# Performance work log

Hardware: AMD Instinct MI355X
Metric: run time of the kernel (lower is better)

Reference implementation:

```python
import jax, jax.numpy as jnp
import numpy as np

D_INNER = 5120
DT_RANK = 160
N_STATE = 16
BATCH = 256


def _softplus_thresh20(x):
    # ttnn.softplus(parameter1=1.0, parameter2=20.0): linear above threshold 20
    return jnp.where(x > 20.0, x, jnp.log1p(jnp.exp(jnp.minimum(x, 20.0))))


def setup_inputs() -> dict:
    key = jax.random.key(0)
    ks = jax.random.split(key, 9)
    x = jax.random.normal(ks[0], (1, 1, BATCH, D_INNER), dtype=jnp.float32)
    # scale weights by 1/sqrt(fan_in) so softplus input is O(1)
    W_dt_low = jax.random.normal(ks[1], (D_INNER, DT_RANK), dtype=jnp.float32) / np.sqrt(D_INNER)
    W_dt = jax.random.normal(ks[2], (DT_RANK, D_INNER), dtype=jnp.float32) / np.sqrt(DT_RANK)
    b_dt = jax.random.normal(ks[3], (D_INNER,), dtype=jnp.float32)
    W_B = jax.random.normal(ks[4], (D_INNER, N_STATE), dtype=jnp.float32) / np.sqrt(D_INNER)
    W_C = jax.random.normal(ks[5], (D_INNER, N_STATE), dtype=jnp.float32) / np.sqrt(D_INNER)
    # A = -exp(A_log): strictly negative, as in the module's preprocess_A
    A = -jnp.exp(0.5 * jax.random.normal(ks[6], (D_INNER, N_STATE), dtype=jnp.float32))
    D = jax.random.normal(ks[7], (D_INNER,), dtype=jnp.float32)
    h0 = 0.1 * jax.random.normal(ks[8], (BATCH, D_INNER, N_STATE), dtype=jnp.float32)
    return {"x": x, "W_dt_low": W_dt_low, "W_dt": W_dt, "b_dt": b_dt,
            "W_B": W_B, "W_C": W_C, "A": A, "D": D, "h0": h0}


def reference(x, W_dt_low, W_dt, b_dt, W_B, W_C, A, D, h0):
    b, d = x.shape[2], x.shape[3]
    xb = x.reshape(b, d)                                  # (B, D)
    # delta = softplus(x @ x_proj_dt @ dt_proj + bias)
    delta = _softplus_thresh20(xb @ W_dt_low @ W_dt + b_dt)   # (B, D)
    Bp = xb @ W_B                                         # (B, N)
    Cp = xb @ W_C                                         # (B, N)
    # discretize: abar = exp(delta * A), bbar = delta * B
    # layout (B, D, N) matches repeat_interleave(delta, n) / repeat(B, d)
    abar = jnp.exp(delta[:, :, None] * A[None, :, :])     # (B, D, N)
    bbar = delta[:, :, None] * Bp[:, None, :]             # (B, D, N)
    h = abar * h0 + bbar * xb[:, :, None]                 # (B, D, N)
    y = jnp.einsum('bdn,bn->bd', h, Cp)                   # reduce over state
    out = xb * D[None, :] + y                             # (B, D)
    return out.reshape(1, 1, b, d)
```

## Files before the change

kernel.cpp:

```cpp
#include <hip/hip_runtime.h>
#include <math.h>

#define D_INNER 5120
#define DT_RANK 160
#define N_STATE 16
#define BATCH   256
#define KTOT    192

#define BGRP    8
#define NBG     (BATCH / BGRP)
#define DDBLK   160
#define NDDB    (D_INNER / DDBLK)
#define SPLIT   32

#define K3_BT   8

#define OFF_T     0
#define SZ_T      (BATCH * KTOT)
#define OFF_P     (OFF_T + SZ_T)
#define SZ_P      (SPLIT * BATCH * KTOT)
#define OFF_SBC   (OFF_P + SZ_P)

__global__ __launch_bounds__(256) void k1_gemm(const float* __restrict__ x,
                                               const float* __restrict__ Wdtlow,
                                               const float* __restrict__ WB,
                                               const float* __restrict__ WC,
                                               float* __restrict__ ws) {
    __shared__ float lds[4 * BGRP * KTOT];
    const int tid  = threadIdx.x;
    const int lane = tid & 63;
    const int wv   = tid >> 6;
    const int b0   = blockIdx.x * BGRP;
    const int ddB  = blockIdx.y * DDBLK;

    float* xs = lds;
    for (int j = tid; j < (BGRP * DDBLK) / 4; j += 256) {
        int i  = j / (DDBLK / 4);
        int c4 = j % (DDBLK / 4);
        float4 v = *(const float4*)(x + (size_t)(b0 + i) * D_INNER + ddB + c4 * 4);
        *(float4*)(xs + i * DDBLK + c4 * 4) = v;
    }
    __syncthreads();

    const int dd0 = wv * 40;
    const float* p0 = Wdtlow + (size_t)(ddB + dd0) * DT_RANK + lane;
    const float* p1 = p0 + 64;
    const float* p2;
    int st2;
    if (lane < 32)      { p2 = p0 + 128;                                          st2 = DT_RANK; }
    else if (lane < 48) { p2 = WB + (size_t)(ddB + dd0) * N_STATE + (lane - 32);  st2 = N_STATE; }
    else                { p2 = WC + (size_t)(ddB + dd0) * N_STATE + (lane - 48);  st2 = N_STATE; }

    float acc0[BGRP], acc1[BGRP], acc2[BGRP];
#pragma unroll
    for (int i = 0; i < BGRP; ++i) { acc0[i] = 0.f; acc1[i] = 0.f; acc2[i] = 0.f; }

#pragma unroll 2
    for (int g = 0; g < 10; ++g) {
        float w0[4], w1[4], w2[4];
#pragma unroll
        for (int u = 0; u < 4; ++u) {
            int dd = g * 4 + u;
            w0[u] = p0[(size_t)dd * DT_RANK];
            w1[u] = p1[(size_t)dd * DT_RANK];
            w2[u] = p2[(size_t)dd * st2];
        }
#pragma unroll
        for (int i = 0; i < BGRP; ++i) {
            float4 xv = *(const float4*)(xs + i * DDBLK + dd0 + g * 4);
            acc0[i] += xv.x * w0[0] + xv.y * w0[1] + xv.z * w0[2] + xv.w * w0[3];
            acc1[i] += xv.x * w1[0] + xv.y * w1[1] + xv.z * w1[2] + xv.w * w1[3];
            acc2[i] += xv.x * w2[0] + xv.y * w2[1] + xv.z * w2[2] + xv.w * w2[3];
        }
    }
    __syncthreads();

#pragma unroll
    for (int i = 0; i < BGRP; ++i) {
        float* r = lds + wv * (BGRP * KTOT) + i * KTOT;
        r[lane]       = acc0[i];
        r[lane + 64]  = acc1[i];
        r[lane + 128] = acc2[i];
    }
    __syncthreads();

    float* P = ws + OFF_P + (size_t)blockIdx.y * (BATCH * KTOT) + (size_t)b0 * KTOT;
#pragma unroll
    for (int r = 0; r < 6; ++r) {
        int idx = tid + r * 256;
        P[idx] = lds[idx] + lds[idx + 1536] + lds[idx + 3072] + lds[idx + 4608];
    }
}

__global__ __launch_bounds__(192) void k2_reduce(float* __restrict__ ws) {
    __shared__ float ts[KTOT];
    const int b   = blockIdx.x;
    const int col = threadIdx.x;
    const float* P = ws + OFF_P + (size_t)b * KTOT + col;
    float a = 0.f;
#pragma unroll
    for (int s = 0; s < SPLIT; ++s) a += P[(size_t)s * (BATCH * KTOT)];
    ws[OFF_T + b * KTOT + col] = a;
    ts[col] = a;
    __syncthreads();
    if (col == 0) {
        float s2 = 0.f;
#pragma unroll
        for (int n = 0; n < N_STATE; ++n) s2 += ts[160 + n] * ts[176 + n];
        ws[OFF_SBC + b] = s2;
    }
}

__global__ __launch_bounds__(256, 4) void k3_fused(const float* __restrict__ Wdt,
                                                   const float* __restrict__ b_dt,
                                                   const float* __restrict__ x,
                                                   const float* __restrict__ A,
                                                   const float* __restrict__ Dv,
                                                   const float* __restrict__ h0,
                                                   const float* __restrict__ ws,
                                                   float* __restrict__ out) {
    const int tid = threadIdx.x;
    const int d   = blockIdx.x * 256 + tid;
    const int b0  = blockIdx.y * K3_BT;
    const float* T  = ws + OFF_T;
    const float* SB = ws + OFF_SBC;

    const float4* hb = (const float4*)(h0 + ((size_t)b0 * D_INNER + d) * N_STATE);
    const size_t  hstride = (size_t)D_INNER * 4;

    float4 hc0 = hb[0], hc1 = hb[1], hc2 = hb[2], hc3 = hb[3];
    const float4* h1p = hb + hstride;
    float4 hn0 = h1p[0], hn1 = h1p[1], hn2 = h1p[2], hn3 = h1p[3];

    float xv[K3_BT];
#pragma unroll
    for (int i = 0; i < K3_BT; ++i) xv[i] = x[(size_t)(b0 + i) * D_INNER + d];

    const float bdt = b_dt[d];
    const float Dd  = Dv[d];
    const float4* a4 = (const float4*)(A + (size_t)d * N_STATE);
    float4 a0 = a4[0], a1 = a4[1], a2 = a4[2], a3 = a4[3];

    float acc[K3_BT] = {0.f, 0.f, 0.f, 0.f, 0.f, 0.f, 0.f, 0.f};
#pragma unroll 4
    for (int k = 0; k < DT_RANK; ++k) {
        float w = Wdt[(size_t)k * D_INNER + d];
#pragma unroll
        for (int i = 0; i < K3_BT; ++i)
            acc[i] += T[(size_t)(b0 + i) * KTOT + k] * w;
    }

#pragma unroll
    for (int i = 0; i < K3_BT; ++i) {
        float4 p0, p1, p2, p3;
        if (i + 2 < K3_BT) {
            const float4* hp = hb + (size_t)(i + 2) * hstride;
            p0 = hp[0]; p1 = hp[1]; p2 = hp[2]; p3 = hp[3];
        }

        const int b = b0 + i;
        const float* Tb = T + (size_t)b * KTOT;

        float v     = acc[i] + bdt;
        float delta = (v > 20.f) ? v : log1pf(__expf(v));
        float sbc   = SB[b];

        float y0, y1, y2, y3;
        y0  = __expf(delta * a0.x) * hc0.x * Tb[176 + 0];
        y0 += __expf(delta * a0.y) * hc0.y * Tb[176 + 1];
        y0 += __expf(delta * a0.z) * hc0.z * Tb[176 + 2];
        y0 += __expf(delta * a0.w) * hc0.w * Tb[176 + 3];
        y1  = __expf(delta * a1.x) * hc1.x * Tb[176 + 4];
        y1 += __expf(delta * a1.y) * hc1.y * Tb[176 + 5];
        y1 += __expf(delta * a1.z) * hc1.z * Tb[176 + 6];
        y1 += __expf(delta * a1.w) * hc1.w * Tb[176 + 7];
        y2  = __expf(delta * a2.x) * hc2.x * Tb[176 + 8];
        y2 += __expf(delta * a2.y) * hc2.y * Tb[176 + 9];
        y2 += __expf(delta * a2.z) * hc2.z * Tb[176 + 10];
        y2 += __expf(delta * a2.w) * hc2.w * Tb[176 + 11];
        y3  = __expf(delta * a3.x) * hc3.x * Tb[176 + 12];
        y3 += __expf(delta * a3.y) * hc3.y * Tb[176 + 13];
        y3 += __expf(delta * a3.z) * hc3.z * Tb[176 + 14];
        y3 += __expf(delta * a3.w) * hc3.w * Tb[176 + 15];

        out[(size_t)b * D_INNER + d] = xv[i] * (Dd + delta * sbc)
                                     + ((y0 + y1) + (y2 + y3));

        if (i < K3_BT - 1) { hc0 = hn0; hc1 = hn1; hc2 = hn2; hc3 = hn3; }
        if (i + 2 < K3_BT) { hn0 = p0;  hn1 = p1;  hn2 = p2;  hn3 = p3;  }
    }
}

extern "C" void kernel_launch(void* const* d_in, const int* in_sizes, int n_in,
                              void* d_out, int out_size, void* d_ws, size_t ws_size,
                              hipStream_t stream) {
    const float* x      = (const float*)d_in[0];
    const float* Wdtlow = (const float*)d_in[1];
    const float* Wdt    = (const float*)d_in[2];
    const float* bdt    = (const float*)d_in[3];
    const float* WB     = (const float*)d_in[4];
    const float* WC     = (const float*)d_in[5];
    const float* A      = (const float*)d_in[6];
    const float* Dv     = (const float*)d_in[7];
    const float* h0     = (const float*)d_in[8];
    float* ws  = (float*)d_ws;
    float* out = (float*)d_out;

    hipLaunchKernelGGL(k1_gemm, dim3(NBG, NDDB), dim3(256), 0, stream,
                       x, Wdtlow, WB, WC, ws);
    hipLaunchKernelGGL(k2_reduce, dim3(BATCH), dim3(192), 0, stream, ws);
    hipLaunchKernelGGL(k3_fused, dim3(D_INNER / 256, BATCH / K3_BT), dim3(256),
                       0, stream, Wdt, bdt, x, A, Dv, h0, ws, out);
}
```

Measured before the change: 182.8 us.

## Split fused delta+scan kernel into separate delta GEMM and streaming scan kernels

Breaks the fused third kernel into two: one computes delta (the low-rank GEMM plus softplus) with 4 batches per block and writes it to workspace, and a second streams h0 with one batch per block to form the output. This is meant to let the h0-bandwidth-bound scan run at higher occupancy without the GEMM's register pressure or the manual prefetch pipeline. In exchange it adds an extra launch and a round trip of a BATCH×D_INNER delta buffer through global memory, and the GEMM now reads the Wdt weights twice as often.

Result: no change. 181.5 us (-0.7%).

```diff
diff --git a/kernel.cpp b/kernel.cpp
--- a/kernel.cpp
+++ b/kernel.cpp
@@ -13,13 +13,14 @@
 #define NDDB    (D_INNER / DDBLK)
 #define SPLIT   32
 
-#define K3_BT   8
+#define K3A_BT  4
 
 #define OFF_T     0
 #define SZ_T      (BATCH * KTOT)
 #define OFF_P     (OFF_T + SZ_T)
 #define SZ_P      (SPLIT * BATCH * KTOT)
 #define OFF_SBC   (OFF_P + SZ_P)
+#define OFF_DELTA (OFF_SBC + BATCH)
 
 __global__ __launch_bounds__(256) void k1_gemm(const float* __restrict__ x,
                                                const float* __restrict__ Wdtlow,
@@ -111,9 +112,33 @@
     }
 }
 
-__global__ __launch_bounds__(256, 4) void k3_fused(const float* __restrict__ Wdt,
-                                                   const float* __restrict__ b_dt,
-                                                   const float* __restrict__ x,
+__global__ __launch_bounds__(256, 8) void k3a_delta(const float* __restrict__ Wdt,
+                                                    const float* __restrict__ b_dt,
+                                                    float* __restrict__ ws) {
+    const int tid = threadIdx.x;
+    const int d   = blockIdx.x * 256 + tid;
+    const int b0  = blockIdx.y * K3A_BT;
+    const float* T = ws + OFF_T;
+
+    float acc[K3A_BT] = {0.f, 0.f, 0.f, 0.f};
+#pragma unroll 8
+    for (int k = 0; k < DT_RANK; ++k) {
+        float w = Wdt[(size_t)k * D_INNER + d];
+#pragma unroll
+        for (int i = 0; i < K3A_BT; ++i)
+            acc[i] += T[(size_t)(b0 + i) * KTOT + k] * w;
+    }
+
+    const float bdt = b_dt[d];
+#pragma unroll
+    for (int i = 0; i < K3A_BT; ++i) {
+        float v     = acc[i] + bdt;
+        float delta = (v > 20.f) ? v : log1pf(__expf(v));
+        ws[OFF_DELTA + (size_t)(b0 + i) * D_INNER + d] = delta;
+    }
+}
+
+__global__ __launch_bounds__(256, 8) void k3b_scan(const float* __restrict__ x,
                                                    const float* __restrict__ A,
                                                    const float* __restrict__ Dv,
                                                    const float* __restrict__ h0,
@@ -121,74 +146,40 @@
                                                    float* __restrict__ out) {
     const int tid = threadIdx.x;
     const int d   = blockIdx.x * 256 + tid;
-    const int b0  = blockIdx.y * K3_BT;
-    const float* T  = ws + OFF_T;
-    const float* SB = ws + OFF_SBC;
-
-    const float4* hb = (const float4*)(h0 + ((size_t)b0 * D_INNER + d) * N_STATE);
-    const size_t  hstride = (size_t)D_INNER * 4;
-
-    float4 hc0 = hb[0], hc1 = hb[1], hc2 = hb[2], hc3 = hb[3];
-    const float4* h1p = hb + hstride;
-    float4 hn0 = h1p[0], hn1 = h1p[1], hn2 = h1p[2], hn3 = h1p[3];
-
-    float xv[K3_BT];
-#pragma unroll
-    for (int i = 0; i < K3_BT; ++i) xv[i] = x[(size_t)(b0 + i) * D_INNER + d];
-
-    const float bdt = b_dt[d];
-    const float Dd  = Dv[d];
+    const int b   = blockIdx.y;
+    const float* Tb = ws + OFF_T + (size_t)b * KTOT;
+
+    const float4* hp = (const float4*)(h0 + ((size_t)b * D_INNER + d) * N_STATE);
+    float4 h0v = hp[0], h1v = hp[1], h2v = hp[2], h3v = hp[3];
+
     const float4* a4 = (const float4*)(A + (size_t)d * N_STATE);
     float4 a0 = a4[0], a1 = a4[1], a2 = a4[2], a3 = a4[3];
 
-    float acc[K3_BT] = {0.f, 0.f, 0.f, 0.f, 0.f, 0.f, 0.f, 0.f};
-#pragma unroll 4
-    for (int k = 0; k < DT_RANK; ++k) {
-        float w = Wdt[(size_t)k * D_INNER + d];
-#pragma unroll
-        for (int i = 0; i < K3_BT; ++i)
-            acc[i] += T[(size_t)(b0 + i) * KTOT + k] * w;
-    }
-
-#pragma unroll
-    for (int i = 0; i < K3_BT; ++i) {
-        float4 p0, p1, p2, p3;
-        if (i + 2 < K3_BT) {
-            const float4* hp = hb + (size_t)(i + 2) * hstride;
-            p0 = hp[0]; p1 = hp[1]; p2 = hp[2]; p3 = hp[3];
-        }
-
-        const int b = b0 + i;
-        const float* Tb = T + (size_t)b * KTOT;
-
-        float v     = acc[i] + bdt;
-        float delta = (v > 20.f) ? v : log1pf(__expf(v));
-        float sbc   = SB[b];
-
-        float y0, y1, y2, y3;
-        y0  = __expf(delta * a0.x) * hc0.x * Tb[176 + 0];
-        y0 += __expf(delta * a0.y) * hc0.y * Tb[176 + 1];
-        y0 += __expf(delta * a0.z) * hc0.z * Tb[176 + 2];
-        y0 += __expf(delta * a0.w) * hc0.w * Tb[176 + 3];
-        y1  = __expf(delta * a1.x) * hc1.x * Tb[176 + 4];
-        y1 += __expf(delta * a1.y) * hc1.y * Tb[176 + 5];
-        y1 += __expf(delta * a1.z) * hc1.z * Tb[176 + 6];
-        y1 += __expf(delta * a1.w) * hc1.w * Tb[176 + 7];
-        y2  = __expf(delta * a2.x) * hc2.x * Tb[176 + 8];
-        y2 += __expf(delta * a2.y) * hc2.y * Tb[176 + 9];
-        y2 += __expf(delta * a2.z) * hc2.z * Tb[176 + 10];
-        y2 += __expf(delta * a2.w) * hc2.w * Tb[176 + 11];
-        y3  = __expf(delta * a3.x) * hc3.x * Tb[176 + 12];
-        y3 += __expf(delta * a3.y) * hc3.y * Tb[176 + 13];
-        y3 += __expf(delta * a3.z) * hc3.z * Tb[176 + 14];
-        y3 += __expf(delta * a3.w) * hc3.w * Tb[176 + 15];
-
-        out[(size_t)b * D_INNER + d] = xv[i] * (Dd + delta * sbc)
-                                     + ((y0 + y1) + (y2 + y3));
-
-        if (i < K3_BT - 1) { hc0 = hn0; hc1 = hn1; hc2 = hn2; hc3 = hn3; }
-        if (i + 2 < K3_BT) { hn0 = p0;  hn1 = p1;  hn2 = p2;  hn3 = p3;  }
-    }
+    const size_t bd = (size_t)b * D_INNER + d;
+    float delta = ws[OFF_DELTA + bd];
+    float xv    = x[bd];
+    float Dd    = Dv[d];
+    float sbc   = ws[OFF_SBC + b];
+
+    float y0, y1, y2, y3;
+    y0  = __expf(delta * a0.x) * h0v.x * Tb[176 + 0];
+    y0 += __expf(delta * a0.y) * h0v.y * Tb[176 + 1];
+    y0 += __expf(delta * a0.z) * h0v.z * Tb[176 + 2];
+    y0 += __expf(delta * a0.w) * h0v.w * Tb[176 + 3];
+    y1  = __expf(delta * a1.x) * h1v.x * Tb[176 + 4];
+    y1 += __expf(delta * a1.y) * h1v.y * Tb[176 + 5];
+    y1 += __expf(delta * a1.z) * h1v.z * Tb[176 + 6];
+    y1 += __expf(delta * a1.w) * h1v.w * Tb[176 + 7];
+    y2  = __expf(delta * a2.x) * h2v.x * Tb[176 + 8];
+    y2 += __expf(delta * a2.y) * h2v.y * Tb[176 + 9];
+    y2 += __expf(delta * a2.z) * h2v.z * Tb[176 + 10];
+    y2 += __expf(delta * a2.w) * h2v.w * Tb[176 + 11];
+    y3  = __expf(delta * a3.x) * h3v.x * Tb[176 + 12];
+    y3 += __expf(delta * a3.y) * h3v.y * Tb[176 + 13];
+    y3 += __expf(delta * a3.z) * h3v.z * Tb[176 + 14];
+    y3 += __expf(delta * a3.w) * h3v.w * Tb[176 + 15];
+
+    out[bd] = xv * (Dd + delta * sbc) + ((y0 + y1) + (y2 + y3));
 }
 
 extern "C" void kernel_launch(void* const* d_in, const int* in_sizes, int n_in,
@@ -209,6 +200,8 @@
     hipLaunchKernelGGL(k1_gemm, dim3(NBG, NDDB), dim3(256), 0, stream,
                        x, Wdtlow, WB, WC, ws);
     hipLaunchKernelGGL(k2_reduce, dim3(BATCH), dim3(192), 0, stream, ws);
-    hipLaunchKernelGGL(k3_fused, dim3(D_INNER / 256, BATCH / K3_BT), dim3(256),
-                       0, stream, Wdt, bdt, x, A, Dv, h0, ws, out);
-}
+    hipLaunchKernelGGL(k3a_delta, dim3(D_INNER / 256, BATCH / K3A_BT), dim3(256),
+                       0, stream, Wdt, bdt, ws);
+    hipLaunchKernelGGL(k3b_scan, dim3(D_INNER / 256, BATCH), dim3(256),
+                       0, stream, x, A, Dv, h0, ws, out);
+}
```
